# Performance work log

Measured on AMD Instinct MI355X. Metric: run time of the kernel, lower is better.

Reference implementation:

```python
import jax, jax.numpy as jnp
import numpy as np
from jax import lax

ITER = 3
SMOOTH = 1.0
W_DICE = 1.0
W_CLDICE = 1.0


def _pool(x, window, is_min):
    # torch max_pool pads with -inf, so -maxpool(-x) is a minpool padded with +inf
    pads = [(k // 2, k // 2) for k in window]
    if is_min:
        return lax.reduce_window(x, jnp.inf, lax.min, window, (1,) * x.ndim, pads)
    return lax.reduce_window(x, -jnp.inf, lax.max, window, (1,) * x.ndim, pads)


def soft_erode(img):
    # min over three axis-aligned 3-wide min-pools (5D NCDHW path)
    p1 = _pool(img, (1, 1, 3, 1, 1), True)
    p2 = _pool(img, (1, 1, 1, 3, 1), True)
    p3 = _pool(img, (1, 1, 1, 1, 3), True)
    return jnp.minimum(jnp.minimum(p1, p2), p3)


def soft_dilate(img):
    return _pool(img, (1, 1, 3, 3, 3), False)


def soft_open(img):
    return soft_dilate(soft_erode(img))


def soft_skel(img, iter_):
    skel = jax.nn.relu(img - soft_open(img))
    for _ in range(iter_):  # small static iteration count
        img = soft_erode(img)
        delta = jax.nn.relu(img - soft_open(img))
        skel = skel + jax.nn.relu(delta - skel * delta)
    return skel


def setup_inputs() -> dict:
    key = jax.random.key(0)
    k1, k2 = jax.random.split(key)
    y_pred = jax.random.normal(k1, (2, 2, 96, 192, 192), dtype=jnp.float32)
    y_true = jax.random.randint(k2, (2, 1, 96, 192, 192), 0, 2, dtype=jnp.int64)
    return {"y_pred": y_pred, "y_true": y_true}


def reference(y_pred, y_true):
    p = jax.nn.softmax(y_pred, axis=1)  # [B,C,D,H,W]
    C = p.shape[1]
    # one-hot scatter along channel dim: y_true [B,1,D,H,W]
    oh = (jnp.arange(C, dtype=y_true.dtype)[None, :, None, None, None] == y_true).astype(p.dtype)
    # soft dice (foreground channels only); note original swaps args but math is symmetric
    inter = jnp.sum((oh * p)[:, 1:])
    dice = 1.0 - (2.0 * inter + SMOOTH) / (jnp.sum(oh[:, 1:]) + jnp.sum(p[:, 1:]) + SMOOTH)
    skel_pred = soft_skel(p, ITER)
    skel_true = soft_skel(oh, ITER)
    tprec = (jnp.sum((skel_pred * oh)[:, 1:]) + SMOOTH) / (jnp.sum(skel_pred[:, 1:]) + SMOOTH)
    tsens = (jnp.sum((skel_true * p)[:, 1:]) + SMOOTH) / (jnp.sum(skel_true[:, 1:]) + SMOOTH)
    cl_dice = 1.0 - 2.0 * (tprec * tsens) / (tprec + tsens)
    return W_DICE * dice + W_CLDICE * cl_dice
```

## Files before the change

### kernel.cpp

```cpp
#include <hip/hip_runtime.h>
#include <hip/hip_fp16.h>
#include <math.h>

#define WD 192
#define HD 192
#define DD 96
#define HW (HD*WD)
#define VOL (DD*HD*WD)

typedef unsigned int u32;
#define ONE1 0x3C00u
#define ONE2 0x3C003C00u
#define W8N (WD/8)
#define EBLOCKS ((W8N*HD*(DD/2))/256)

#define NBP (2*(VOL/8/256))
#define DLTH 192
#define NBD ((W8N*HD*(DD/2))/DLTH)

struct EOffs  { long long in[4]; long long out[4]; };
struct DLOffs { long long rows[4]; long long prev[4]; long long prod[4];
                long long wgt[4]; int cid[4]; };

__device__ __forceinline__ float sigf(float l) { return 1.0f / (1.0f + __expf(-l)); }

__device__ __forceinline__ u32 pmin(u32 a, u32 b) {
    u32 lo = ((a & 0xffffu) < (b & 0xffffu)) ? (a & 0xffffu) : (b & 0xffffu);
    u32 hi = ((a >> 16) < (b >> 16)) ? (a & 0xffff0000u) : (b & 0xffff0000u);
    return lo | hi;
}
__device__ __forceinline__ u32 pmax(u32 a, u32 b) {
    u32 lo = ((a & 0xffffu) > (b & 0xffffu)) ? (a & 0xffffu) : (b & 0xffffu);
    u32 hi = ((a >> 16) > (b >> 16)) ? (a & 0xffff0000u) : (b & 0xffff0000u);
    return lo | hi;
}
__device__ __forceinline__ uint4 pmin4(uint4 a, uint4 b) {
    return make_uint4(pmin(a.x,b.x), pmin(a.y,b.y), pmin(a.z,b.z), pmin(a.w,b.w));
}
__device__ __forceinline__ uint4 pmax4(uint4 a, uint4 b) {
    return make_uint4(pmax(a.x,b.x), pmax(a.y,b.y), pmax(a.z,b.z), pmax(a.w,b.w));
}
__device__ __forceinline__ uint4 ld4f(const __half* p, bool v, u32 fill) {
    if (v) return *(const uint4*)p;
    return make_uint4(fill, fill, fill, fill);
}
__device__ __forceinline__ uint4 shl8(uint4 r, u32 lh) {
    return make_uint4((r.x << 16) | (lh & 0xffffu), (r.y << 16) | (r.x >> 16),
                      (r.z << 16) | (r.y >> 16),    (r.w << 16) | (r.z >> 16));
}
__device__ __forceinline__ uint4 shr8(uint4 r, u32 rh) {
    return make_uint4((r.x >> 16) | (r.y << 16), (r.y >> 16) | (r.z << 16),
                      (r.z >> 16) | (r.w << 16), (r.w >> 16) | (rh << 16));
}
__device__ __forceinline__ u32 pack2f(float a, float b) {
    return (u32)__half_as_ushort(__float2half_rn(a)) |
           ((u32)__half_as_ushort(__float2half_rn(b)) << 16);
}
__device__ __forceinline__ void unp8(uint4 q, float* f) {
    u32 a[4] = { q.x, q.y, q.z, q.w };
    #pragma unroll
    for (int j = 0; j < 4; ++j) {
        f[2*j]   = __half2float(__ushort_as_half((unsigned short)(a[j] & 0xffffu)));
        f[2*j+1] = __half2float(__ushort_as_half((unsigned short)(a[j] >> 16)));
    }
}

__global__ void __launch_bounds__(256)
prep_kernel(__half* vols, const float* __restrict__ yp, const int* __restrict__ yt,
            float* __restrict__ pprt) {
    const int b = blockIdx.z;
    const float* pb = yp + (size_t)b * (2 * (size_t)VOL);
    const int*   tb = yt + (size_t)b * (size_t)VOL;
    __half* pv = vols + (size_t)b * (size_t)VOL;
    __half* ov = vols + (size_t)(2 + b) * (size_t)VOL;

    const int i = blockIdx.x * 256 + threadIdx.x;
    const int idx = i * 8;

    float4 a0 = *(const float4*)(pb + idx);
    float4 a1 = *(const float4*)(pb + idx + 4);
    float4 c0 = *(const float4*)(pb + (size_t)VOL + idx);
    float4 c1 = *(const float4*)(pb + (size_t)VOL + idx + 4);
    int4   t0 = *(const int4*)(tb + idx);
    int4   t1 = *(const int4*)(tb + idx + 4);

    float p[8] = { sigf(c0.x-a0.x), sigf(c0.y-a0.y), sigf(c0.z-a0.z), sigf(c0.w-a0.w),
                   sigf(c1.x-a1.x), sigf(c1.y-a1.y), sigf(c1.z-a1.z), sigf(c1.w-a1.w) };
    int   t[8] = { t0.x, t0.y, t0.z, t0.w, t1.x, t1.y, t1.z, t1.w };

    uint4 pq = make_uint4(pack2f(p[0],p[1]), pack2f(p[2],p[3]),
                          pack2f(p[4],p[5]), pack2f(p[6],p[7]));
    u32 om[4];
    #pragma unroll
    for (int j = 0; j < 4; ++j)
        om[j] = ((t[2*j] == 1) ? ONE1 : 0u) | ((t[2*j+1] == 1) ? (ONE1 << 16) : 0u);
    *(uint4*)(pv + idx) = pq;
    *(uint4*)(ov + idx) = make_uint4(om[0], om[1], om[2], om[3]);

    float ds_p = 0.f, ds_o = 0.f, ds_i = 0.f;
    #pragma unroll
    for (int j = 0; j < 8; ++j) {
        ds_p += p[j];
        if (t[j] == 1) { ds_o += 1.f; ds_i += p[j]; }
    }
    #pragma unroll
    for (int off = 32; off > 0; off >>= 1) {
        ds_p += __shfl_down(ds_p, off);
        ds_o += __shfl_down(ds_o, off);
        ds_i += __shfl_down(ds_i, off);
    }
    __shared__ float sA[4], sB[4], sC[4];
    int tid = threadIdx.x, wid = tid >> 6, lane = tid & 63;
    if (lane == 0) { sA[wid] = ds_p; sB[wid] = ds_o; sC[wid] = ds_i; }
    __syncthreads();
    if (tid == 0) {
        const int bid = blockIdx.z * gridDim.x + blockIdx.x;
        pprt[bid*3 + 0] = sA[0]+sA[1]+sA[2]+sA[3];
        pprt[bid*3 + 1] = sB[0]+sB[1]+sB[2]+sB[3];
        pprt[bid*3 + 2] = sC[0]+sC[1]+sC[2]+sC[3];
    }
}

__global__ void __launch_bounds__(256)
e_kernel(__half* base, EOffs o) {
    const int zc = blockIdx.z;
    const __half* src = base + o.in[zc];
    __half* dst = base + o.out[zc];

    const int i  = blockIdx.x * 256 + threadIdx.x;
    const int w8 = i % W8N;
    const int h  = (i / W8N) % HD;
    const int z  = (i / (W8N * HD)) * 2;
    const int idx = (z * HD + h) * WD + w8 * 8;

    uint4 c0 = *(const uint4*)(src + idx);
    uint4 c1 = *(const uint4*)(src + idx + HW);
    uint4 zm  = ld4f(src + idx - HW, z > 0, ONE2);
    uint4 zp  = ld4f(src + idx + 2*HW, z + 2 < DD, ONE2);
    uint4 u0  = ld4f(src + idx - WD, h > 0, ONE2);
    uint4 u1  = ld4f(src + idx + HW - WD, h > 0, ONE2);
    uint4 dn0 = ld4f(src + idx + WD, h < HD - 1, ONE2);
    uint4 dn1 = ld4f(src + idx + HW + WD, h < HD - 1, ONE2);
    const unsigned short* ss = (const unsigned short*)src;
    u32 l0 = (w8 > 0) ? ss[idx - 1] : ONE1;
    u32 l1 = (w8 > 0) ? ss[idx + HW - 1] : ONE1;
    u32 r0 = (w8 < W8N-1) ? ss[idx + 8] : ONE1;
    u32 r1 = (w8 < W8N-1) ? ss[idx + HW + 8] : ONE1;

    uint4 wm0 = pmin4(pmin4(shl8(c0, l0), c0), shr8(c0, r0));
    uint4 wm1 = pmin4(pmin4(shl8(c1, l1), c1), shr8(c1, r1));
    uint4 o0 = pmin4(pmin4(wm0, u0), pmin4(dn0, pmin4(zm, c1)));
    uint4 o1 = pmin4(pmin4(wm1, u1), pmin4(dn1, pmin4(c0, zp)));
    *(uint4*)(dst + idx) = o0;
    *(uint4*)(dst + idx + HW) = o1;
}

template<int MODE>
__global__ void __launch_bounds__(DLTH)
dl_kernel(__half* base, DLOffs o, float* __restrict__ fprt) {
    const int zc = blockIdx.z;
    const __half* R  = base + o.rows[zc];
    const __half* PV = base + o.prev[zc];

    const int tid = threadIdx.x;
    const int i  = blockIdx.x * DLTH + tid;
    const int w8 = i % W8N;
    const int h  = (i / W8N) % HD;
    const int z  = (i / (W8N * HD)) * 2;
    const int idx = (z * HD + h) * WD + w8 * 8;

    const bool rok0 = h > 0, rok2 = h < HD - 1;
    const bool zok0 = z > 0, zok3 = z + 2 < DD;
    const uint4 zer = make_uint4(0u,0u,0u,0u);

    uint4 M0 = zer, M1 = zer;
    #pragma unroll
    for (int zz = 0; zz < 4; ++zz) {
        const bool zv = (zz == 0) ? zok0 : (zz == 3) ? zok3 : true;
        const int off = ((z - 1 + zz) * HD + h) * WD + w8 * 8;
        uint4 r0 = ld4f(R + off - WD, zv && rok0, 0u);
        uint4 r1 = ld4f(R + off,      zv,         0u);
        uint4 r2 = ld4f(R + off + WD, zv && rok2, 0u);
        uint4 vmax = pmax4(pmax4(r0, r1), r2);
        if (zz <= 2) M0 = pmax4(M0, vmax);
        if (zz >= 1) M1 = pmax4(M1, vmax);
    }

    __shared__ u32 eL[DLTH], eR[DLTH];
    eL[tid] = (M0.x & 0xffffu) | (M1.x << 16);
    eR[tid] = (M0.w >> 16) | (M1.w & 0xffff0000u);
    __syncthreads();
    u32 lh = (w8 > 0)       ? eR[tid - 1] : 0u;
    u32 rh = (w8 < W8N - 1) ? eL[tid + 1] : 0u;

    uint4 D0 = pmax4(pmax4(shl8(M0, lh & 0xffffu), M0), shr8(M0, rh & 0xffffu));
    uint4 D1 = pmax4(pmax4(shl8(M1, lh >> 16),     M1), shr8(M1, rh >> 16));

    float dv0[8], dv1[8], pc0[8], pc1[8];
    unp8(D0, dv0); unp8(D1, dv1);
    unp8(*(const uint4*)(PV + idx), pc0);
    unp8(*(const uint4*)(PV + idx + HW), pc1);
    float f0[8], f1[8];
    #pragma unroll
    for (int j = 0; j < 8; ++j) {
        f0[j] = 1.f - fmaxf(pc0[j] - dv0[j], 0.f);
        f1[j] = 1.f - fmaxf(pc1[j] - dv1[j], 0.f);
    }

    __half* PR = base + o.prod[zc];
    if constexpr (MODE == 0) {
        *(uint4*)(PR + idx) = make_uint4(pack2f(f0[0],f0[1]), pack2f(f0[2],f0[3]),
                                         pack2f(f0[4],f0[5]), pack2f(f0[6],f0[7]));
        *(uint4*)(PR + idx + HW) = make_uint4(pack2f(f1[0],f1[1]), pack2f(f1[2],f1[3]),
                                              pack2f(f1[4],f1[5]), pack2f(f1[6],f1[7]));
    } else if constexpr (MODE == 1) {
        float pr0[8], pr1[8];
        unp8(*(const uint4*)(PR + idx), pr0);
        unp8(*(const uint4*)(PR + idx + HW), pr1);
        #pragma unroll
        for (int j = 0; j < 8; ++j) { f0[j] *= pr0[j]; f1[j] *= pr1[j]; }
        *(uint4*)(PR + idx) = make_uint4(pack2f(f0[0],f0[1]), pack2f(f0[2],f0[3]),
                                         pack2f(f0[4],f0[5]), pack2f(f0[6],f0[7]));
        *(uint4*)(PR + idx + HW) = make_uint4(pack2f(f1[0],f1[1]), pack2f(f1[2],f1[3]),
                                              pack2f(f1[4],f1[5]), pack2f(f1[6],f1[7]));
    } else {
        const __half* WV = base + o.wgt[zc];
        float pr0[8], pr1[8], W0[8], W1[8];
        unp8(*(const uint4*)(PR + idx), pr0);
        unp8(*(const uint4*)(PR + idx + HW), pr1);
        unp8(*(const uint4*)(WV + idx), W0);
        unp8(*(const uint4*)(WV + idx + HW), W1);
        float s_sum = 0.f, w_sum = 0.f;
        #pragma unroll
        for (int j = 0; j < 8; ++j) {
            float a = 1.f - pr0[j] * f0[j];
            float b = 1.f - pr1[j] * f1[j];
            s_sum += a + b;
            w_sum += a * W0[j] + b * W1[j];
        }
        #pragma unroll
        for (int off = 32; off > 0; off >>= 1) {
            s_sum += __shfl_down(s_sum, off);
            w_sum += __shfl_down(w_sum, off);
        }
        __shared__ float rs[3], rw[3];
        int wid = tid >> 6, lane = tid & 63;
        if (lane == 0) { rs[wid] = s_sum; rw[wid] = w_sum; }
        __syncthreads();
        if (tid == 0) {
            float* dst = fprt + ((size_t)o.cid[zc] * NBD + blockIdx.x) * 2;
            dst[0] = rs[0] + rs[1] + rs[2];
            dst[1] = rw[0] + rw[1] + rw[2];
        }
    }
}

__global__ void __launch_bounds__(256)
finalize_kernel(const float* __restrict__ pprt, const float* __restrict__ fprt,
                float* __restrict__ out) {
    const int tid = threadIdx.x;
    double l[7] = {0,0,0,0,0,0,0};
    for (int i = tid; i < NBP; i += 256) {
        l[0] += (double)pprt[i*3 + 0];
        l[1] += (double)pprt[i*3 + 1];
        l[2] += (double)pprt[i*3 + 2];
    }
    for (int i = tid; i < 4*NBD; i += 256) {
        int grp = (i / NBD) >> 1;
        l[3 + grp*2 + 0] += (double)fprt[i*2 + 0];
        l[3 + grp*2 + 1] += (double)fprt[i*2 + 1];
    }
    __shared__ double sd[256];
    double r[7];
    for (int k = 0; k < 7; ++k) {
        sd[tid] = l[k];
        __syncthreads();
        for (int s = 128; s > 0; s >>= 1) {
            if (tid < s) sd[tid] += sd[tid + s];
            __syncthreads();
        }
        r[k] = sd[0];
        __syncthreads();
    }
    if (tid == 0) {
        double sum_p = r[0], sum_oh = r[1], inter = r[2];
        double sp_s = r[3], sp_w = r[4];
        double st_s = r[5], st_w = r[6];
        double dice  = 1.0 - (2.0 * inter + 1.0) / (sum_oh + sum_p + 1.0);
        double tprec = (sp_w + 1.0) / (sp_s + 1.0);
        double tsens = (st_w + 1.0) / (st_s + 1.0);
        double cl    = 1.0 - 2.0 * (tprec * tsens) / (tprec + tsens);
        out[0] = (float)(dice + cl);
    }
}

extern "C" void kernel_launch(void* const* d_in, const int* in_sizes, int n_in,
                              void* d_out, int out_size, void* d_ws, size_t ws_size,
                              hipStream_t stream) {
    const float* y_pred = (const float*)d_in[0];
    const int*   y_true = (const int*)d_in[1];
    float* out = (float*)d_out;

    char* ws = (char*)d_ws;
    float* pprt = (float*)ws;
    float* fprt = pprt + 3*NBP;
    __half* vols = (__half*)(ws + 131072);

    const long long V = VOL;
    const long long SRC[4] = { 0, V, 2*V, 3*V };
    const long long WGT[4] = { 2*V, 3*V, 0, V };

    const bool wide = ws_size >= (size_t)131072 + 20ull * (size_t)VOL * 2ull;

    prep_kernel<<<dim3(VOL/8/256, 1, 2), 256, 0, stream>>>(vols, y_pred, y_true, pprt);

    if (wide) {
        long long E0[4], E1[4], E2[4], PR[4];
        for (int c = 0; c < 4; ++c) {
            E0[c] = 4*V + 4LL*c*V; E1[c] = E0[c] + V; E2[c] = E0[c] + 2*V; PR[c] = E0[c] + 3*V;
        }
        dim3 eg(EBLOCKS, 1, 4);
        dim3 dg(NBD, 1, 4);
        EOffs e1o = {{SRC[0],SRC[1],SRC[2],SRC[3]}, {E0[0],E0[1],E0[2],E0[3]}};
        e_kernel<<<eg, 256, 0, stream>>>(vols, e1o);
        DLOffs d1 = {{E0[0],E0[1],E0[2],E0[3]}, {SRC[0],SRC[1],SRC[2],SRC[3]},
                     {PR[0],PR[1],PR[2],PR[3]}, {0,0,0,0}, {0,1,2,3}};
        dl_kernel<0><<<dg, DLTH, 0, stream>>>(vols, d1, fprt);
        EOffs e2o = {{E0[0],E0[1],E0[2],E0[3]}, {E1[0],E1[1],E1[2],E1[3]}};
        e_kernel<<<eg, 256, 0, stream>>>(vols, e2o);
        DLOffs d2 = {{E1[0],E1[1],E1[2],E1[3]}, {E0[0],E0[1],E0[2],E0[3]},
                     {PR[0],PR[1],PR[2],PR[3]}, {0,0,0,0}, {0,1,2,3}};
        dl_kernel<1><<<dg, DLTH, 0, stream>>>(vols, d2, fprt);
        EOffs e3o = {{E1[0],E1[1],E1[2],E1[3]}, {E2[0],E2[1],E2[2],E2[3]}};
        e_kernel<<<eg, 256, 0, stream>>>(vols, e3o);
        DLOffs d3 = {{E2[0],E2[1],E2[2],E2[3]}, {E1[0],E1[1],E1[2],E1[3]},
                     {PR[0],PR[1],PR[2],PR[3]}, {0,0,0,0}, {0,1,2,3}};
        dl_kernel<1><<<dg, DLTH, 0, stream>>>(vols, d3, fprt);
        EOffs e4o = {{E2[0],E2[1],E2[2],E2[3]}, {E0[0],E0[1],E0[2],E0[3]}};
        e_kernel<<<eg, 256, 0, stream>>>(vols, e4o);
        DLOffs d4 = {{E0[0],E0[1],E0[2],E0[3]}, {E2[0],E2[1],E2[2],E2[3]},
                     {PR[0],PR[1],PR[2],PR[3]}, {WGT[0],WGT[1],WGT[2],WGT[3]}, {0,1,2,3}};
        dl_kernel<2><<<dg, DLTH, 0, stream>>>(vols, d4, fprt);
    } else {
        long long E0 = 4*V, E1 = 5*V, E2 = 6*V, PR = 7*V;
        dim3 eg(EBLOCKS, 1, 1);
        dim3 dg(NBD, 1, 1);
        for (int c = 0; c < 4; ++c) {
            EOffs e1o = {{SRC[c],0,0,0}, {E0,0,0,0}};
            e_kernel<<<eg, 256, 0, stream>>>(vols, e1o);
            DLOffs d1 = {{E0,0,0,0}, {SRC[c],0,0,0}, {PR,0,0,0}, {0,0,0,0}, {c,0,0,0}};
            dl_kernel<0><<<dg, DLTH, 0, stream>>>(vols, d1, fprt);
            EOffs e2o = {{E0,0,0,0}, {E1,0,0,0}};
            e_kernel<<<eg, 256, 0, stream>>>(vols, e2o);
            DLOffs d2 = {{E1,0,0,0}, {E0,0,0,0}, {PR,0,0,0}, {0,0,0,0}, {c,0,0,0}};
            dl_kernel<1><<<dg, DLTH, 0, stream>>>(vols, d2, fprt);
            EOffs e3o = {{E1,0,0,0}, {E2,0,0,0}};
            e_kernel<<<eg, 256, 0, stream>>>(vols, e3o);
            DLOffs d3 = {{E2,0,0,0}, {E1,0,0,0}, {PR,0,0,0}, {0,0,0,0}, {c,0,0,0}};
            dl_kernel<1><<<dg, DLTH, 0, stream>>>(vols, d3, fprt);
            EOffs e4o = {{E2,0,0,0}, {E0,0,0,0}};
            e_kernel<<<eg, 256, 0, stream>>>(vols, e4o);
            DLOffs d4 = {{E0,0,0,0}, {E2,0,0,0}, {PR,0,0,0}, {WGT[c],0,0,0}, {c,0,0,0}};
            dl_kernel<2><<<dg, DLTH, 0, stream>>>(vols, d4, fprt);
        }
    }

    finalize_kernel<<<1, 256, 0, stream>>>(pprt, fprt, out);
}
```

Baseline: 165.3 us.

## Fuse pairs of dilate-skeleton stages into one kernel processing two erosion levels

Replaces four dilate/product kernels per channel with two fused kernels. Each fused kernel computes the 3x3x3 max-pool of two consecutive erosion levels and reuses the center rows of the first as the previous volume for the second. This removes one full read-modify-write of the product buffer and two kernel launches per chain. In exchange each kernel carries more registers and shared memory, which may lower occupancy, and the erosion kernels are reordered so two erosions run back to back before each fused kernel.

```diff
diff --git a/kernel.cpp b/kernel.cpp
--- a/kernel.cpp
+++ b/kernel.cpp
@@ -19,8 +19,8 @@
 #define NBD ((W8N*HD*(DD/2))/DLTH)
 
 struct EOffs  { long long in[4]; long long out[4]; };
-struct DLOffs { long long rows[4]; long long prev[4]; long long prod[4];
-                long long wgt[4]; int cid[4]; };
+struct DLOffs { long long rA[4]; long long rB[4]; long long prev[4];
+                long long prod[4]; long long wgt[4]; int cid[4]; };
 
 __device__ __forceinline__ float sigf(float l) { return 1.0f / (1.0f + __expf(-l)); }
 
@@ -62,6 +62,26 @@
     for (int j = 0; j < 4; ++j) {
         f[2*j]   = __half2float(__ushort_as_half((unsigned short)(a[j] & 0xffffu)));
         f[2*j+1] = __half2float(__ushort_as_half((unsigned short)(a[j] >> 16)));
+    }
+}
+
+__device__ __forceinline__ void colmax(const __half* R, int z, int h, int w8,
+                                       bool rok0, bool rok2, bool zok0, bool zok3,
+                                       uint4& M0, uint4& M1, uint4& c0, uint4& c1) {
+    const uint4 zer = make_uint4(0u,0u,0u,0u);
+    M0 = zer; M1 = zer;
+    #pragma unroll
+    for (int zz = 0; zz < 4; ++zz) {
+        const bool zv = (zz == 0) ? zok0 : (zz == 3) ? zok3 : true;
+        const int off = ((z - 1 + zz) * HD + h) * WD + w8 * 8;
+        uint4 r0 = ld4f(R + off - WD, zv && rok0, 0u);
+        uint4 r1 = ld4f(R + off,      zv,         0u);
+        uint4 r2 = ld4f(R + off + WD, zv && rok2, 0u);
+        if (zz == 1) c0 = r1;
+        if (zz == 2) c1 = r1;
+        uint4 vmax = pmax4(pmax4(r0, r1), r2);
+        if (zz <= 2) M0 = pmax4(M0, vmax);
+        if (zz >= 1) M1 = pmax4(M1, vmax);
     }
 }
 
@@ -157,9 +177,10 @@
 
 template<int MODE>
 __global__ void __launch_bounds__(DLTH)
-dl_kernel(__half* base, DLOffs o, float* __restrict__ fprt) {
+dl2_kernel(__half* base, DLOffs o, float* __restrict__ fprt) {
     const int zc = blockIdx.z;
-    const __half* R  = base + o.rows[zc];
+    const __half* RA = base + o.rA[zc];
+    const __half* RB = base + o.rB[zc];
     const __half* PV = base + o.prev[zc];
 
     const int tid = threadIdx.x;
@@ -171,54 +192,42 @@
 
     const bool rok0 = h > 0, rok2 = h < HD - 1;
     const bool zok0 = z > 0, zok3 = z + 2 < DD;
-    const uint4 zer = make_uint4(0u,0u,0u,0u);
-
-    uint4 M0 = zer, M1 = zer;
-    #pragma unroll
-    for (int zz = 0; zz < 4; ++zz) {
-        const bool zv = (zz == 0) ? zok0 : (zz == 3) ? zok3 : true;
-        const int off = ((z - 1 + zz) * HD + h) * WD + w8 * 8;
-        uint4 r0 = ld4f(R + off - WD, zv && rok0, 0u);
-        uint4 r1 = ld4f(R + off,      zv,         0u);
-        uint4 r2 = ld4f(R + off + WD, zv && rok2, 0u);
-        uint4 vmax = pmax4(pmax4(r0, r1), r2);
-        if (zz <= 2) M0 = pmax4(M0, vmax);
-        if (zz >= 1) M1 = pmax4(M1, vmax);
-    }
-
-    __shared__ u32 eL[DLTH], eR[DLTH];
-    eL[tid] = (M0.x & 0xffffu) | (M1.x << 16);
-    eR[tid] = (M0.w >> 16) | (M1.w & 0xffff0000u);
+
+    uint4 M0a, M1a, ca0, ca1;
+    colmax(RA, z, h, w8, rok0, rok2, zok0, zok3, M0a, M1a, ca0, ca1);
+    uint4 M0b, M1b, cb0, cb1;
+    colmax(RB, z, h, w8, rok0, rok2, zok0, zok3, M0b, M1b, cb0, cb1);
+
+    __shared__ u32 eLa[DLTH], eRa[DLTH], eLb[DLTH], eRb[DLTH];
+    eLa[tid] = (M0a.x & 0xffffu) | (M1a.x << 16);
+    eRa[tid] = (M0a.w >> 16) | (M1a.w & 0xffff0000u);
+    eLb[tid] = (M0b.x & 0xffffu) | (M1b.x << 16);
+    eRb[tid] = (M0b.w >> 16) | (M1b.w & 0xffff0000u);
     __syncthreads();
-    u32 lh = (w8 > 0)       ? eR[tid - 1] : 0u;
-    u32 rh = (w8 < W8N - 1) ? eL[tid + 1] : 0u;
-
-    uint4 D0 = pmax4(pmax4(shl8(M0, lh & 0xffffu), M0), shr8(M0, rh & 0xffffu));
-    uint4 D1 = pmax4(pmax4(shl8(M1, lh >> 16),     M1), shr8(M1, rh >> 16));
-
-    float dv0[8], dv1[8], pc0[8], pc1[8];
-    unp8(D0, dv0); unp8(D1, dv1);
-    unp8(*(const uint4*)(PV + idx), pc0);
-    unp8(*(const uint4*)(PV + idx + HW), pc1);
+    u32 lha = (w8 > 0)       ? eRa[tid - 1] : 0u;
+    u32 rha = (w8 < W8N - 1) ? eLa[tid + 1] : 0u;
+    u32 lhb = (w8 > 0)       ? eRb[tid - 1] : 0u;
+    u32 rhb = (w8 < W8N - 1) ? eLb[tid + 1] : 0u;
+
+    uint4 D0a = pmax4(pmax4(shl8(M0a, lha & 0xffffu), M0a), shr8(M0a, rha & 0xffffu));
+    uint4 D1a = pmax4(pmax4(shl8(M1a, lha >> 16),     M1a), shr8(M1a, rha >> 16));
+    uint4 D0b = pmax4(pmax4(shl8(M0b, lhb & 0xffffu), M0b), shr8(M0b, rhb & 0xffffu));
+    uint4 D1b = pmax4(pmax4(shl8(M1b, lhb >> 16),     M1b), shr8(M1b, rhb >> 16));
+
+    float da0[8], da1[8], db0[8], db1[8], pv0[8], pv1[8], cc0[8], cc1[8];
+    unp8(D0a, da0); unp8(D1a, da1); unp8(D0b, db0); unp8(D1b, db1);
+    unp8(*(const uint4*)(PV + idx), pv0);
+    unp8(*(const uint4*)(PV + idx + HW), pv1);
+    unp8(ca0, cc0); unp8(ca1, cc1);
     float f0[8], f1[8];
     #pragma unroll
     for (int j = 0; j < 8; ++j) {
-        f0[j] = 1.f - fmaxf(pc0[j] - dv0[j], 0.f);
-        f1[j] = 1.f - fmaxf(pc1[j] - dv1[j], 0.f);
+        f0[j] = (1.f - fmaxf(pv0[j] - da0[j], 0.f)) * (1.f - fmaxf(cc0[j] - db0[j], 0.f));
+        f1[j] = (1.f - fmaxf(pv1[j] - da1[j], 0.f)) * (1.f - fmaxf(cc1[j] - db1[j], 0.f));
     }
 
     __half* PR = base + o.prod[zc];
     if constexpr (MODE == 0) {
-        *(uint4*)(PR + idx) = make_uint4(pack2f(f0[0],f0[1]), pack2f(f0[2],f0[3]),
-                                         pack2f(f0[4],f0[5]), pack2f(f0[6],f0[7]));
-        *(uint4*)(PR + idx + HW) = make_uint4(pack2f(f1[0],f1[1]), pack2f(f1[2],f1[3]),
-                                              pack2f(f1[4],f1[5]), pack2f(f1[6],f1[7]));
-    } else if constexpr (MODE == 1) {
-        float pr0[8], pr1[8];
-        unp8(*(const uint4*)(PR + idx), pr0);
-        unp8(*(const uint4*)(PR + idx + HW), pr1);
-        #pragma unroll
-        for (int j = 0; j < 8; ++j) { f0[j] *= pr0[j]; f1[j] *= pr1[j]; }
         *(uint4*)(PR + idx) = make_uint4(pack2f(f0[0],f0[1]), pack2f(f0[2],f0[3]),
                                          pack2f(f0[4],f0[5]), pack2f(f0[6],f0[7]));
         *(uint4*)(PR + idx + HW) = make_uint4(pack2f(f1[0],f1[1]), pack2f(f1[2],f1[3]),
@@ -323,24 +332,20 @@
         dim3 dg(NBD, 1, 4);
         EOffs e1o = {{SRC[0],SRC[1],SRC[2],SRC[3]}, {E0[0],E0[1],E0[2],E0[3]}};
         e_kernel<<<eg, 256, 0, stream>>>(vols, e1o);
-        DLOffs d1 = {{E0[0],E0[1],E0[2],E0[3]}, {SRC[0],SRC[1],SRC[2],SRC[3]},
-                     {PR[0],PR[1],PR[2],PR[3]}, {0,0,0,0}, {0,1,2,3}};
-        dl_kernel<0><<<dg, DLTH, 0, stream>>>(vols, d1, fprt);
         EOffs e2o = {{E0[0],E0[1],E0[2],E0[3]}, {E1[0],E1[1],E1[2],E1[3]}};
         e_kernel<<<eg, 256, 0, stream>>>(vols, e2o);
-        DLOffs d2 = {{E1[0],E1[1],E1[2],E1[3]}, {E0[0],E0[1],E0[2],E0[3]},
-                     {PR[0],PR[1],PR[2],PR[3]}, {0,0,0,0}, {0,1,2,3}};
-        dl_kernel<1><<<dg, DLTH, 0, stream>>>(vols, d2, fprt);
+        DLOffs dA = {{E0[0],E0[1],E0[2],E0[3]}, {E1[0],E1[1],E1[2],E1[3]},
+                     {SRC[0],SRC[1],SRC[2],SRC[3]}, {PR[0],PR[1],PR[2],PR[3]},
+                     {0,0,0,0}, {0,1,2,3}};
+        dl2_kernel<0><<<dg, DLTH, 0, stream>>>(vols, dA, fprt);
         EOffs e3o = {{E1[0],E1[1],E1[2],E1[3]}, {E2[0],E2[1],E2[2],E2[3]}};
         e_kernel<<<eg, 256, 0, stream>>>(vols, e3o);
-        DLOffs d3 = {{E2[0],E2[1],E2[2],E2[3]}, {E1[0],E1[1],E1[2],E1[3]},
-                     {PR[0],PR[1],PR[2],PR[3]}, {0,0,0,0}, {0,1,2,3}};
-        dl_kernel<1><<<dg, DLTH, 0, stream>>>(vols, d3, fprt);
         EOffs e4o = {{E2[0],E2[1],E2[2],E2[3]}, {E0[0],E0[1],E0[2],E0[3]}};
         e_kernel<<<eg, 256, 0, stream>>>(vols, e4o);
-        DLOffs d4 = {{E0[0],E0[1],E0[2],E0[3]}, {E2[0],E2[1],E2[2],E2[3]},
-                     {PR[0],PR[1],PR[2],PR[3]}, {WGT[0],WGT[1],WGT[2],WGT[3]}, {0,1,2,3}};
-        dl_kernel<2><<<dg, DLTH, 0, stream>>>(vols, d4, fprt);
+        DLOffs dB = {{E2[0],E2[1],E2[2],E2[3]}, {E0[0],E0[1],E0[2],E0[3]},
+                     {E1[0],E1[1],E1[2],E1[3]}, {PR[0],PR[1],PR[2],PR[3]},
+                     {WGT[0],WGT[1],WGT[2],WGT[3]}, {0,1,2,3}};
+        dl2_kernel<1><<<dg, DLTH, 0, stream>>>(vols, dB, fprt);
     } else {
         long long E0 = 4*V, E1 = 5*V, E2 = 6*V, PR = 7*V;
         dim3 eg(EBLOCKS, 1, 1);
@@ -348,20 +353,18 @@
         for (int c = 0; c < 4; ++c) {
             EOffs e1o = {{SRC[c],0,0,0}, {E0,0,0,0}};
             e_kernel<<<eg, 256, 0, stream>>>(vols, e1o);
-            DLOffs d1 = {{E0,0,0,0}, {SRC[c],0,0,0}, {PR,0,0,0}, {0,0,0,0}, {c,0,0,0}};
-            dl_kernel<0><<<dg, DLTH, 0, stream>>>(vols, d1, fprt);
             EOffs e2o = {{E0,0,0,0}, {E1,0,0,0}};
             e_kernel<<<eg, 256, 0, stream>>>(vols, e2o);
-            DLOffs d2 = {{E1,0,0,0}, {E0,0,0,0}, {PR,0,0,0}, {0,0,0,0}, {c,0,0,0}};
-            dl_kernel<1><<<dg, DLTH, 0, stream>>>(vols, d2, fprt);
+            DLOffs dA = {{E0,0,0,0}, {E1,0,0,0}, {SRC[c],0,0,0}, {PR,0,0,0},
+                         {0,0,0,0}, {c,0,0,0}};
+            dl2_kernel<0><<<dg, DLTH, 0, stream>>>(vols, dA, fprt);
             EOffs e3o = {{E1,0,0,0}, {E2,0,0,0}};
             e_kernel<<<eg, 256, 0, stream>>>(vols, e3o);
-            DLOffs d3 = {{E2,0,0,0}, {E1,0,0,0}, {PR,0,0,0}, {0,0,0,0}, {c,0,0,0}};
-            dl_kernel<1><<<dg, DLTH, 0, stream>>>(vols, d3, fprt);
             EOffs e4o = {{E2,0,0,0}, {E0,0,0,0}};
             e_kernel<<<eg, 256, 0, stream>>>(vols, e4o);
-            DLOffs d4 = {{E0,0,0,0}, {E2,0,0,0}, {PR,0,0,0}, {WGT[c],0,0,0}, {c,0,0,0}};
-            dl_kernel<2><<<dg, DLTH, 0, stream>>>(vols, d4, fprt);
+            DLOffs dB = {{E2,0,0,0}, {E0,0,0,0}, {E1,0,0,0}, {PR,0,0,0},
+                         {WGT[c],0,0,0}, {c,0,0,0}};
+            dl2_kernel<1><<<dg, DLTH, 0, stream>>>(vols, dB, fprt);
         }
     }
 
```

After: 143.4 us. 13.2% less time.
